# Optimization experiments

Measured on AMD Instinct MI355X. Metric: run time of the kernel, lower is better.

Reference implementation:

```python
import jax, jax.numpy as jnp
import numpy as np
import math

CHUNK = 256
NUM_HEADS = 4
EPS = 1e-5


def setup_inputs() -> dict:
    key = jax.random.key(0)
    ks = jax.random.split(key, 12)
    B, N, F = 4, 2048, 256
    x = jax.random.normal(ks[0], (B, N, F), dtype=jnp.float32)
    adj_matrix = jax.random.randint(ks[1], (N, N), 0, 2, dtype=jnp.int32)
    s = 1.0 / math.sqrt(F)
    Wq = jax.random.normal(ks[2], (F, F), dtype=jnp.float32) * s
    bq = jnp.zeros((F,), dtype=jnp.float32)
    Wk = jax.random.normal(ks[3], (F, F), dtype=jnp.float32) * s
    bk = jnp.zeros((F,), dtype=jnp.float32)
    Wv = jax.random.normal(ks[4], (F, F), dtype=jnp.float32) * s
    bv = jnp.zeros((F,), dtype=jnp.float32)
    Wo = jax.random.normal(ks[5], (F, F), dtype=jnp.float32) * s
    bo = jnp.zeros((F,), dtype=jnp.float32)
    gamma = jnp.ones((F,), dtype=jnp.float32)
    beta = jnp.zeros((F,), dtype=jnp.float32)
    return {"x": x, "adj_matrix": adj_matrix, "Wq": Wq, "bq": bq, "Wk": Wk,
            "bk": bk, "Wv": Wv, "bv": bv, "Wo": Wo, "bo": bo,
            "gamma": gamma, "beta": beta}


def reference(x, adj_matrix, Wq, bq, Wk, bk, Wv, bv, Wo, bo, gamma, beta):
    B, N, Fin = x.shape
    H = NUM_HEADS
    Dout = Wq.shape[0]
    Dh = Dout // H
    Nc = N // CHUNK  # number of key chunks

    # projections -> [B, H, N, Dh]
    q = (x @ Wq.T + bq).reshape(B, N, H, Dh).transpose(0, 2, 1, 3)
    k = (x @ Wk.T + bk).reshape(B, N, H, Dh).transpose(0, 2, 1, 3)
    v = (x @ Wv.T + bv).reshape(B, N, H, Dh).transpose(0, 2, 1, 3)

    # key/value chunks: [B, H, Nc, CHUNK, Dh]
    kc = k.reshape(B, H, Nc, CHUNK, Dh)
    vc = v.reshape(B, H, Nc, CHUNK, Dh)

    # scores per key chunk: [B, H, N, Nc, CHUNK]
    scores = jnp.einsum('bhnd,bhjcd->bhnjc', q, kc) / jnp.sqrt(
        jnp.asarray(Dh, dtype=q.dtype))
    scores = jnp.clip(scores, -10.0, 10.0)
    # adjacency mask, chunked along keys: [1, 1, N, Nc, CHUNK]
    mask = adj_matrix.reshape(N, Nc, CHUNK)[None, None]
    scores = jnp.where(mask == 0, jnp.asarray(-10.0, scores.dtype), scores)

    # FAITHFUL quirk: softmax is taken per key chunk (last axis only) and the
    # per-chunk contexts are SUMMED -> total attention mass per query is Nc.
    attn = jax.nn.softmax(scores, axis=-1)
    ctx = jnp.einsum('bhnjc,bhjcd->bhnd', attn, vc)  # sum over chunks j

    ctx = ctx.transpose(0, 2, 1, 3).reshape(B, N, Dout)
    out = ctx @ Wo.T + bo
    out = out + x  # residual (in_features == out_features)

    mu = jnp.mean(out, axis=-1, keepdims=True)
    var = jnp.mean(jnp.square(out - mu), axis=-1, keepdims=True)
    out = (out - mu) * jax.lax.rsqrt(var + EPS) * gamma + beta
    return out
```

## Files before the change

kernel.cpp:

```cpp
#include <hip/hip_runtime.h>
#include <math.h>

#define B_     4
#define N_     2048
#define F_     256
#define H_     4
#define DH     64
#define BN     8192
#define SP     72
#define SPO2   264
#define SPW    264

#define QSCALE 0.18033688011112042f
#define CLIP   14.426950408889634f

typedef _Float16 f16;
typedef _Float16 half8  __attribute__((ext_vector_type(8)));
typedef _Float16 half4v __attribute__((ext_vector_type(4)));
typedef float    floatx4 __attribute__((ext_vector_type(4)));
typedef unsigned long long u64;

__global__ __launch_bounds__(256) void prep_kernel(
    const int* __restrict__ adj, u64* __restrict__ P,
    const float* __restrict__ x,  f16* __restrict__ xh,
    const float* __restrict__ Wq, f16* __restrict__ Wqh,
    const float* __restrict__ Wk, f16* __restrict__ Wkh,
    const float* __restrict__ Wv, f16* __restrict__ Wvh,
    const float* __restrict__ Wo, f16* __restrict__ Woh)
{
    const int bid = blockIdx.x;
    if (bid < 16384) {
        const int row   = bid >> 3;
        const int chunk = bid & 7;
        const int wave  = threadIdx.x >> 6, lane = threadIdx.x & 63;
        const int key   = chunk * 256 + wave * 64 + lane;
        u64 m = __ballot(adj[(size_t)row * N_ + key] != 0);
        if (lane == 0) P[(size_t)row * 32 + chunk * 4 + wave] = m;
        return;
    }
    const float* src; f16* dst; int base;
    if      (bid < 16448) { src = Wo; dst = Woh; base = (bid - 16384) * 1024; }
    else if (bid < 16512) { src = Wq; dst = Wqh; base = (bid - 16448) * 1024; }
    else if (bid < 16576) { src = Wk; dst = Wkh; base = (bid - 16512) * 1024; }
    else if (bid < 16640) { src = Wv; dst = Wvh; base = (bid - 16576) * 1024; }
    else                  { src = x;  dst = xh;  base = (bid - 16640) * 1024; }
    const int idx = base + threadIdx.x * 4;
    float4 v = *(const float4*)(src + idx);
    half4v h; h[0] = (f16)v.x; h[1] = (f16)v.y; h[2] = (f16)v.z; h[3] = (f16)v.w;
    *(half4v*)(dst + idx) = h;
}

__global__ __launch_bounds__(512) void proj_mfma(
    const f16* __restrict__ xh,
    const f16* __restrict__ Wqh, const f16* __restrict__ Wkh, const f16* __restrict__ Wvh,
    const float* __restrict__ bq, const float* __restrict__ bk, const float* __restrict__ bv,
    f16* __restrict__ Qh, f16* __restrict__ Kh, f16* __restrict__ Vt)
{
    const int which = blockIdx.y;
    const f16*   W    = which == 0 ? Wqh : which == 1 ? Wkh : Wvh;
    const float* bias = which == 0 ? bq  : which == 1 ? bk  : bv;

    const int r0 = blockIdx.x * 64;
    const int tid  = threadIdx.x;
    const int wave = tid >> 6, lane = tid & 63;
    const int quad = lane >> 4, l16 = lane & 15;
    const int rw = wave & 3, cw = wave >> 2;

    __shared__ f16 smem[(64 + 256) * SP];
    f16* xs = smem;
    f16* wt = smem + 64 * SP;

    floatx4 zz = {0.f, 0.f, 0.f, 0.f};
    floatx4 acc[8] = {zz, zz, zz, zz, zz, zz, zz, zz};

    const int xrow = tid >> 3, xseg = (tid & 7) * 8;
    const int wrow = tid >> 1, wh = (tid & 1) * 32;

    for (int f0 = 0; f0 < F_; f0 += 64) {
        const f16* xsrc = xh + (size_t)(r0 + xrow) * F_ + f0 + xseg;
        const f16* wsrc = W  + (size_t)wrow * F_ + f0 + wh;
        float4 xa  = *(const float4*)(xsrc);
        float4 wa0 = *(const float4*)(wsrc),      wa1 = *(const float4*)(wsrc + 8);
        float4 wa2 = *(const float4*)(wsrc + 16), wa3 = *(const float4*)(wsrc + 24);
        __syncthreads();
        *(float4*)&xs[xrow * SP + xseg]   = xa;
        *(float4*)&wt[wrow * SP + wh]      = wa0;
        *(float4*)&wt[wrow * SP + wh + 8]  = wa1;
        *(float4*)&wt[wrow * SP + wh + 16] = wa2;
        *(float4*)&wt[wrow * SP + wh + 24] = wa3;
        __syncthreads();
        half8 a0 = *(const half8*)&xs[(rw * 16 + l16) * SP + quad * 8];
        half8 a1 = *(const half8*)&xs[(rw * 16 + l16) * SP + 32 + quad * 8];
#pragma unroll
        for (int ot = 0; ot < 8; ot++) {
            const int o = cw * 128 + ot * 16 + l16;
            half8 b0 = *(const half8*)&wt[o * SP + quad * 8];
            half8 b1 = *(const half8*)&wt[o * SP + 32 + quad * 8];
            acc[ot] = __builtin_amdgcn_mfma_f32_16x16x32_f16(a0, b0, acc[ot], 0, 0, 0);
            acc[ot] = __builtin_amdgcn_mfma_f32_16x16x32_f16(a1, b1, acc[ot], 0, 0, 0);
        }
    }

    const int bb = r0 >> 11, nn0 = r0 & (N_ - 1);

    if (which == 2) {
#pragma unroll
        for (int ot = 0; ot < 8; ot++) {
            const int o  = cw * 128 + ot * 16 + l16;
            const int hy = o >> 6, dh = o & 63;
            const float bv_ = bias[o];
            half4v h4;
#pragma unroll
            for (int r = 0; r < 4; r++) h4[r] = (f16)(acc[ot][r] + bv_);
            *(half4v*)(Vt + (((size_t)bb * H_ + hy) * DH + dh) * N_
                          + nn0 + rw * 16 + quad * 4) = h4;
        }
    } else {
        const float scl = (which == 0) ? QSCALE : 1.0f;
        f16* dst = which == 0 ? Qh : Kh;
        __syncthreads();
        f16* outb = smem;
#pragma unroll
        for (int ot = 0; ot < 8; ot++) {
            const int o = cw * 128 + ot * 16 + l16;
            const float bv_ = bias[o];
#pragma unroll
            for (int r = 0; r < 4; r++)
                outb[(rw * 16 + quad * 4 + r) * SPO2 + o] =
                    (f16)((acc[ot][r] + bv_) * scl);
        }
        __syncthreads();
        const int grow = tid >> 3, gseg = tid & 7;
        const int hh = gseg >> 1, dcol = (gseg & 1) * 32;
        f16* g = dst + (((size_t)bb * H_ + hh) * N_ + nn0 + grow) * DH + dcol;
        const f16* s = &outb[grow * SPO2 + gseg * 32];
#pragma unroll
        for (int k = 0; k < 4; k++)
            *(float4*)(g + k * 8) = *(const float4*)(s + k * 8);
    }
}

__global__ __launch_bounds__(256) void attn_mfma(
    const f16* __restrict__ Qh, const f16* __restrict__ Kh,
    const f16* __restrict__ Vt, const u64* __restrict__ Padj,
    f16* __restrict__ CTXP)
{
    const int nt = blockIdx.x & 15;
    const int sp = blockIdx.x >> 4;
    const int qb = nt * 128;
    const int h  = blockIdx.y;
    const int b  = blockIdx.z;
    const int bh = b * H_ + h;
    const int tid  = threadIdx.x;
    const int wave = tid >> 6, lane = tid & 63;
    const int quad = lane >> 4, l16 = lane & 15;

    __shared__ f16 QPs[128 * SP];
    __shared__ f16 Ks[64 * SP];
    __shared__ f16 Vs[64 * SP];

    {
        const int qrow = tid >> 1, qhalf = (tid & 1) * 32;
        const f16* src = Qh + ((size_t)bh * N_ + qb + qrow) * DH + qhalf;
#pragma unroll
        for (int k = 0; k < 4; k++)
            *(float4*)&QPs[qrow * SP + qhalf + k * 8] = *(const float4*)(src + k * 8);
    }
    __syncthreads();
    const half8 qf0a = *(const half8*)&QPs[(wave * 32 + l16) * SP + quad * 8];
    const half8 qf1a = *(const half8*)&QPs[(wave * 32 + l16) * SP + 32 + quad * 8];
    const half8 qf0b = *(const half8*)&QPs[(wave * 32 + 16 + l16) * SP + quad * 8];
    const half8 qf1b = *(const half8*)&QPs[(wave * 32 + 16 + l16) * SP + 32 + quad * 8];
    f16* Ps = QPs + wave * 32 * SP;

    const int qgA = qb + wave * 32 + l16;
    const int qgB = qgA + 16;
    const u64* arowA = Padj + (size_t)qgA * 32;
    const u64* arowB = Padj + (size_t)qgB * 32;

    floatx4 zz = {0.f, 0.f, 0.f, 0.f};
    floatx4 totA[4] = {zz, zz, zz, zz}, totB[4] = {zz, zz, zz, zz};

    const int kvr = tid >> 2, kvs = (tid & 3) * 16;

    for (int ci = 0; ci < 2; ci++) {
        const int c = sp * 2 + ci;
        floatx4 chA[4] = {zz, zz, zz, zz}, chB[4] = {zz, zz, zz, zz};
        float rsA = 0.f, rsB = 0.f;

        for (int kt = 0; kt < 4; kt++) {
            const int k0 = c * 256 + kt * 64;
            const f16* ksrc = Kh + ((size_t)bh * N_ + k0 + kvr) * DH + kvs;
            const f16* vsrc = Vt + ((size_t)bh * DH + kvr) * N_ + k0 + kvs;
            float4 ka0 = *(const float4*)(ksrc), ka1 = *(const float4*)(ksrc + 8);
            float4 va0 = *(const float4*)(vsrc), va1 = *(const float4*)(vsrc + 8);
            __syncthreads();
            *(float4*)&Ks[kvr * SP + kvs]     = ka0;
            *(float4*)&Ks[kvr * SP + kvs + 8] = ka1;
            *(float4*)&Vs[kvr * SP + kvs]     = va0;
            *(float4*)&Vs[kvr * SP + kvs + 8] = va1;
            __syncthreads();

            const u64 awA = arowA[k0 >> 6];
            const u64 awB = arowB[k0 >> 6];
            float rA = 0.f, rB = 0.f;
#pragma unroll
            for (int m = 0; m < 4; m++) {
                half8 a0 = *(const half8*)&Ks[(m * 16 + l16) * SP + quad * 8];
                half8 a1 = *(const half8*)&Ks[(m * 16 + l16) * SP + 32 + quad * 8];
                floatx4 sA = zz, sB = zz;
                sA = __builtin_amdgcn_mfma_f32_16x16x32_f16(a0, qf0a, sA, 0, 0, 0);
                sA = __builtin_amdgcn_mfma_f32_16x16x32_f16(a1, qf1a, sA, 0, 0, 0);
                sB = __builtin_amdgcn_mfma_f32_16x16x32_f16(a0, qf0b, sB, 0, 0, 0);
                sB = __builtin_amdgcn_mfma_f32_16x16x32_f16(a1, qf1b, sB, 0, 0, 0);
                const unsigned int nibA = (unsigned int)(awA >> (m * 16 + quad * 4)) & 0xFu;
                const unsigned int nibB = (unsigned int)(awB >> (m * 16 + quad * 4)) & 0xFu;
                half4v pA, pB;
#pragma unroll
                for (int r = 0; r < 4; r++) {
                    float svA = fminf(fmaxf(sA[r], -CLIP), CLIP);
                    svA = ((nibA >> r) & 1u) ? svA : -CLIP;
                    const float eA = __builtin_amdgcn_exp2f(svA);
                    rA += eA; pA[r] = (f16)eA;
                    float svB = fminf(fmaxf(sB[r], -CLIP), CLIP);
                    svB = ((nibB >> r) & 1u) ? svB : -CLIP;
                    const float eB = __builtin_amdgcn_exp2f(svB);
                    rB += eB; pB[r] = (f16)eB;
                }
                *(half4v*)&Ps[l16 * SP + m * 16 + quad * 4]        = pA;
                *(half4v*)&Ps[(16 + l16) * SP + m * 16 + quad * 4] = pB;
            }
            rA += __shfl_xor(rA, 16); rA += __shfl_xor(rA, 32); rsA += rA;
            rB += __shfl_xor(rB, 16); rB += __shfl_xor(rB, 32); rsB += rB;

            const half8 pA0 = *(const half8*)&Ps[l16 * SP + quad * 8];
            const half8 pA1 = *(const half8*)&Ps[l16 * SP + 32 + quad * 8];
            const half8 pB0 = *(const half8*)&Ps[(16 + l16) * SP + quad * 8];
            const half8 pB1 = *(const half8*)&Ps[(16 + l16) * SP + 32 + quad * 8];
#pragma unroll
            for (int m = 0; m < 4; m++) {
                half8 va8 = *(const half8*)&Vs[(m * 16 + l16) * SP + quad * 8];
                half8 vb8 = *(const half8*)&Vs[(m * 16 + l16) * SP + 32 + quad * 8];
                chA[m] = __builtin_amdgcn_mfma_f32_16x16x32_f16(va8, pA0, chA[m], 0, 0, 0);
                chA[m] = __builtin_amdgcn_mfma_f32_16x16x32_f16(vb8, pA1, chA[m], 0, 0, 0);
                chB[m] = __builtin_amdgcn_mfma_f32_16x16x32_f16(va8, pB0, chB[m], 0, 0, 0);
                chB[m] = __builtin_amdgcn_mfma_f32_16x16x32_f16(vb8, pB1, chB[m], 0, 0, 0);
            }
        }

        const float invA = 1.0f / rsA, invB = 1.0f / rsB;
#pragma unroll
        for (int m = 0; m < 4; m++)
#pragma unroll
            for (int r = 0; r < 4; r++) {
                totA[m][r] += chA[m][r] * invA;
                totB[m][r] += chB[m][r] * invB;
            }
    }

    f16* dstA = CTXP + (((size_t)sp * B_ + b) * N_ + qgA) * F_ + h * DH;
    f16* dstB = CTXP + (((size_t)sp * B_ + b) * N_ + qgB) * F_ + h * DH;
#pragma unroll
    for (int m = 0; m < 4; m++) {
        half4v hA, hB;
#pragma unroll
        for (int r = 0; r < 4; r++) { hA[r] = (f16)totA[m][r]; hB[r] = (f16)totB[m][r]; }
        *(half4v*)&dstA[m * 16 + quad * 4] = hA;
        *(half4v*)&dstB[m * 16 + quad * 4] = hB;
    }
}

__global__ __launch_bounds__(256) void out_mfma(
    const f16* __restrict__ CTXP, const float* __restrict__ x,
    const f16* __restrict__ Woh, const float* __restrict__ bo,
    const float* __restrict__ gamma, const float* __restrict__ beta,
    float* __restrict__ out)
{
    const int n0 = blockIdx.x * 16;
    const int tid  = threadIdx.x;
    const int wave = tid >> 6, lane = tid & 63;
    const int quad = lane >> 4, l16 = lane & 15;
    const int wrow = tid >> 2, wseg = tid & 3;

    __shared__ f16 cs[16 * SPW];
    __shared__ f16 wtile[256 * SP];
    __shared__ float red0[4][16], red1[4][16];

    {
        const int row = tid >> 4, c0 = (tid & 15) * 16;
        const size_t S = (size_t)BN * F_;
        const f16* p = CTXP + (size_t)(n0 + row) * F_ + c0;
#pragma unroll
        for (int g = 0; g < 2; g++) {
            half8 s0 = *(const half8*)(p + g * 8);
            half8 s1 = *(const half8*)(p + S + g * 8);
            half8 s2 = *(const half8*)(p + 2 * S + g * 8);
            half8 s3 = *(const half8*)(p + 3 * S + g * 8);
            half8 o;
#pragma unroll
            for (int e = 0; e < 8; e++)
                o[e] = (f16)(((float)s0[e] + (float)s1[e]) + ((float)s2[e] + (float)s3[e]));
            *(half8*)&cs[row * SPW + c0 + g * 8] = o;
        }
    }

    floatx4 zz = {0.f, 0.f, 0.f, 0.f};
    floatx4 acc[4] = {zz, zz, zz, zz};

#pragma unroll
    for (int f0 = 0; f0 < F_; f0 += 64) {
        __syncthreads();
#pragma unroll
        for (int rr = 0; rr < 4; rr++) {
            const int o = rr * 64 + wrow;
            const f16* src = Woh + (size_t)o * F_ + f0 + wseg * 16;
            *(float4*)&wtile[o * SP + wseg * 16]     = *(const float4*)(src);
            *(float4*)&wtile[o * SP + wseg * 16 + 8] = *(const float4*)(src + 8);
        }
        __syncthreads();
        half8 a0 = *(const half8*)&cs[l16 * SPW + f0 + quad * 8];
        half8 a1 = *(const half8*)&cs[l16 * SPW + f0 + 32 + quad * 8];
#pragma unroll
        for (int ot = 0; ot < 4; ot++) {
            const int o = wave * 64 + ot * 16 + l16;
            half8 b0 = *(const half8*)&wtile[o * SP + quad * 8];
            half8 b1 = *(const half8*)&wtile[o * SP + 32 + quad * 8];
            acc[ot] = __builtin_amdgcn_mfma_f32_16x16x32_f16(a0, b0, acc[ot], 0, 0, 0);
            acc[ot] = __builtin_amdgcn_mfma_f32_16x16x32_f16(a1, b1, acc[ot], 0, 0, 0);
        }
    }

#pragma unroll
    for (int ot = 0; ot < 4; ot++) {
        const int o = wave * 64 + ot * 16 + l16;
        const float bo_ = bo[o];
#pragma unroll
        for (int r = 0; r < 4; r++)
            acc[ot][r] += bo_ + x[(size_t)(n0 + quad * 4 + r) * F_ + o];
    }

#pragma unroll
    for (int r = 0; r < 4; r++) {
        float s = (acc[0][r] + acc[1][r]) + (acc[2][r] + acc[3][r]);
        float q = (acc[0][r] * acc[0][r] + acc[1][r] * acc[1][r]) +
                  (acc[2][r] * acc[2][r] + acc[3][r] * acc[3][r]);
        s += __shfl_xor(s, 1); q += __shfl_xor(q, 1);
        s += __shfl_xor(s, 2); q += __shfl_xor(q, 2);
        s += __shfl_xor(s, 4); q += __shfl_xor(q, 4);
        s += __shfl_xor(s, 8); q += __shfl_xor(q, 8);
        if (l16 == 0) { red0[wave][quad * 4 + r] = s; red1[wave][quad * 4 + r] = q; }
    }
    __syncthreads();

#pragma unroll
    for (int r = 0; r < 4; r++) {
        const int rr = quad * 4 + r;
        const float S  = (red0[0][rr] + red0[1][rr]) + (red0[2][rr] + red0[3][rr]);
        const float Q2 = (red1[0][rr] + red1[1][rr]) + (red1[2][rr] + red1[3][rr]);
        const float mu  = S * (1.0f / F_);
        const float var = Q2 * (1.0f / F_) - mu * mu;
        const float inv = rsqrtf(var + 1e-5f);
#pragma unroll
        for (int ot = 0; ot < 4; ot++) {
            const int o = wave * 64 + ot * 16 + l16;
            out[(size_t)(n0 + rr) * F_ + o] =
                (acc[ot][r] - mu) * inv * gamma[o] + beta[o];
        }
    }
}

extern "C" void kernel_launch(void* const* d_in, const int* in_sizes, int n_in,
                              void* d_out, int out_size, void* d_ws, size_t ws_size,
                              hipStream_t stream)
{
    const float* x     = (const float*)d_in[0];
    const int*   adj   = (const int*)  d_in[1];
    const float* Wq    = (const float*)d_in[2];
    const float* bq    = (const float*)d_in[3];
    const float* Wk    = (const float*)d_in[4];
    const float* bk    = (const float*)d_in[5];
    const float* Wv    = (const float*)d_in[6];
    const float* bv    = (const float*)d_in[7];
    const float* Wo    = (const float*)d_in[8];
    const float* bo    = (const float*)d_in[9];
    const float* gamma = (const float*)d_in[10];
    const float* beta  = (const float*)d_in[11];
    float* out = (float*)d_out;

    float* ws = (float*)d_ws;
    f16*   CTXP = (f16*)(ws);
    f16*   Qh   = (f16*)(ws + 4194304);
    f16*   Kh   = (f16*)(ws + 5242880);
    f16*   Vt   = (f16*)(ws + 6291456);
    u64*   Padj = (u64*)(ws + 7340032);
    f16*   Woh  = (f16*)(ws + 7471104);
    f16*   xh   = CTXP;
    f16*   Wqh  = (f16*)(ws + 1048576);
    f16*   Wkh  = (f16*)(ws + 1081344);
    f16*   Wvh  = (f16*)(ws + 1114112);

    hipLaunchKernelGGL(prep_kernel, dim3(18688), dim3(256), 0, stream,
                       adj, Padj, x, xh, Wq, Wqh, Wk, Wkh, Wv, Wvh, Wo, Woh);
    hipLaunchKernelGGL(proj_mfma, dim3(BN / 64, 3), dim3(512), 0, stream,
                       xh, Wqh, Wkh, Wvh, bq, bk, bv, Qh, Kh, Vt);
    hipLaunchKernelGGL(attn_mfma, dim3(64, H_, B_), dim3(256), 0, stream,
                       Qh, Kh, Vt, Padj, CTXP);
    hipLaunchKernelGGL(out_mfma, dim3(BN / 16), dim3(256), 0, stream,
                       CTXP, x, Woh, bo, gamma, beta, out);
}
```

Measured before the change: 163.4 us.

## Fuse prep into projection kernel and split attention into one chunk per block

```diff
diff --git a/kernel.cpp b/kernel.cpp
--- a/kernel.cpp
+++ b/kernel.cpp
@@ -20,48 +20,46 @@
 typedef float    floatx4 __attribute__((ext_vector_type(4)));
 typedef unsigned long long u64;
 
-__global__ __launch_bounds__(256) void prep_kernel(
-    const int* __restrict__ adj, u64* __restrict__ P,
-    const float* __restrict__ x,  f16* __restrict__ xh,
-    const float* __restrict__ Wq, f16* __restrict__ Wqh,
-    const float* __restrict__ Wk, f16* __restrict__ Wkh,
-    const float* __restrict__ Wv, f16* __restrict__ Wvh,
-    const float* __restrict__ Wo, f16* __restrict__ Woh)
+__device__ __forceinline__ half8 cvt8(float4 a, float4 b) {
+    half8 h;
+    h[0] = (f16)a.x; h[1] = (f16)a.y; h[2] = (f16)a.z; h[3] = (f16)a.w;
+    h[4] = (f16)b.x; h[5] = (f16)b.y; h[6] = (f16)b.z; h[7] = (f16)b.w;
+    return h;
+}
+
+__global__ __launch_bounds__(512) void proj_fused(
+    const float* __restrict__ x,
+    const float* __restrict__ Wq, const float* __restrict__ Wk, const float* __restrict__ Wv,
+    const float* __restrict__ bq, const float* __restrict__ bk, const float* __restrict__ bv,
+    const int* __restrict__ adj, u64* __restrict__ Padj,
+    const float* __restrict__ Wo, f16* __restrict__ Woh,
+    f16* __restrict__ Qh, f16* __restrict__ Kh, f16* __restrict__ Vt)
 {
     const int bid = blockIdx.x;
-    if (bid < 16384) {
-        const int row   = bid >> 3;
-        const int chunk = bid & 7;
-        const int wave  = threadIdx.x >> 6, lane = threadIdx.x & 63;
-        const int key   = chunk * 256 + wave * 64 + lane;
+    const int tid = threadIdx.x;
+
+    if (bid >= 416) {
+        const int idx = bid - 416;
+        const int row = idx >> 2, seg = idx & 3;
+        const int wave = tid >> 6, lane = tid & 63;
+        const int key = seg * 512 + wave * 64 + lane;
         u64 m = __ballot(adj[(size_t)row * N_ + key] != 0);
-        if (lane == 0) P[(size_t)row * 32 + chunk * 4 + wave] = m;
+        if (lane == 0) Padj[(size_t)row * 32 + seg * 8 + wave] = m;
         return;
     }
-    const float* src; f16* dst; int base;
-    if      (bid < 16448) { src = Wo; dst = Woh; base = (bid - 16384) * 1024; }
-    else if (bid < 16512) { src = Wq; dst = Wqh; base = (bid - 16448) * 1024; }
-    else if (bid < 16576) { src = Wk; dst = Wkh; base = (bid - 16512) * 1024; }
-    else if (bid < 16640) { src = Wv; dst = Wvh; base = (bid - 16576) * 1024; }
-    else                  { src = x;  dst = xh;  base = (bid - 16640) * 1024; }
-    const int idx = base + threadIdx.x * 4;
-    float4 v = *(const float4*)(src + idx);
-    half4v h; h[0] = (f16)v.x; h[1] = (f16)v.y; h[2] = (f16)v.z; h[3] = (f16)v.w;
-    *(half4v*)(dst + idx) = h;
-}
-
-__global__ __launch_bounds__(512) void proj_mfma(
-    const f16* __restrict__ xh,
-    const f16* __restrict__ Wqh, const f16* __restrict__ Wkh, const f16* __restrict__ Wvh,
-    const float* __restrict__ bq, const float* __restrict__ bk, const float* __restrict__ bv,
-    f16* __restrict__ Qh, f16* __restrict__ Kh, f16* __restrict__ Vt)
-{
-    const int which = blockIdx.y;
-    const f16*   W    = which == 0 ? Wqh : which == 1 ? Wkh : Wvh;
-    const float* bias = which == 0 ? bq  : which == 1 ? bk  : bv;
-
-    const int r0 = blockIdx.x * 64;
-    const int tid  = threadIdx.x;
+    if (bid >= 384) {
+        const int idx = (bid - 384) * 2048 + tid * 4;
+        float4 v = *(const float4*)(Wo + idx);
+        half4v h; h[0] = (f16)v.x; h[1] = (f16)v.y; h[2] = (f16)v.z; h[3] = (f16)v.w;
+        *(half4v*)(Woh + idx) = h;
+        return;
+    }
+
+    const int which = bid >> 7;
+    const float* W    = which == 0 ? Wq : which == 1 ? Wk : Wv;
+    const float* bias = which == 0 ? bq : which == 1 ? bk : bv;
+
+    const int r0 = (bid & 127) * 64;
     const int wave = tid >> 6, lane = tid & 63;
     const int quad = lane >> 4, l16 = lane & 15;
     const int rw = wave & 3, cw = wave >> 2;
@@ -77,17 +75,19 @@
     const int wrow = tid >> 1, wh = (tid & 1) * 32;
 
     for (int f0 = 0; f0 < F_; f0 += 64) {
-        const f16* xsrc = xh + (size_t)(r0 + xrow) * F_ + f0 + xseg;
-        const f16* wsrc = W  + (size_t)wrow * F_ + f0 + wh;
-        float4 xa  = *(const float4*)(xsrc);
-        float4 wa0 = *(const float4*)(wsrc),      wa1 = *(const float4*)(wsrc + 8);
-        float4 wa2 = *(const float4*)(wsrc + 16), wa3 = *(const float4*)(wsrc + 24);
-        __syncthreads();
-        *(float4*)&xs[xrow * SP + xseg]   = xa;
-        *(float4*)&wt[wrow * SP + wh]      = wa0;
-        *(float4*)&wt[wrow * SP + wh + 8]  = wa1;
-        *(float4*)&wt[wrow * SP + wh + 16] = wa2;
-        *(float4*)&wt[wrow * SP + wh + 24] = wa3;
+        const float* xsrc = x + (size_t)(r0 + xrow) * F_ + f0 + xseg;
+        const float* wsrc = W + (size_t)wrow * F_ + f0 + wh;
+        float4 xa0 = *(const float4*)(xsrc), xa1 = *(const float4*)(xsrc + 4);
+        float4 w0 = *(const float4*)(wsrc),      w1 = *(const float4*)(wsrc + 4);
+        float4 w2 = *(const float4*)(wsrc + 8),  w3 = *(const float4*)(wsrc + 12);
+        float4 w4 = *(const float4*)(wsrc + 16), w5 = *(const float4*)(wsrc + 20);
+        float4 w6 = *(const float4*)(wsrc + 24), w7 = *(const float4*)(wsrc + 28);
+        __syncthreads();
+        *(half8*)&xs[xrow * SP + xseg]     = cvt8(xa0, xa1);
+        *(half8*)&wt[wrow * SP + wh]       = cvt8(w0, w1);
+        *(half8*)&wt[wrow * SP + wh + 8]   = cvt8(w2, w3);
+        *(half8*)&wt[wrow * SP + wh + 16]  = cvt8(w4, w5);
+        *(half8*)&wt[wrow * SP + wh + 24]  = cvt8(w6, w7);
         __syncthreads();
         half8 a0 = *(const half8*)&xs[(rw * 16 + l16) * SP + quad * 8];
         half8 a1 = *(const half8*)&xs[(rw * 16 + l16) * SP + 32 + quad * 8];
@@ -179,92 +179,82 @@
     const u64* arowB = Padj + (size_t)qgB * 32;
 
     floatx4 zz = {0.f, 0.f, 0.f, 0.f};
-    floatx4 totA[4] = {zz, zz, zz, zz}, totB[4] = {zz, zz, zz, zz};
+    floatx4 chA[4] = {zz, zz, zz, zz}, chB[4] = {zz, zz, zz, zz};
+    float rsA = 0.f, rsB = 0.f;
 
     const int kvr = tid >> 2, kvs = (tid & 3) * 16;
 
-    for (int ci = 0; ci < 2; ci++) {
-        const int c = sp * 2 + ci;
-        floatx4 chA[4] = {zz, zz, zz, zz}, chB[4] = {zz, zz, zz, zz};
-        float rsA = 0.f, rsB = 0.f;
-
-        for (int kt = 0; kt < 4; kt++) {
-            const int k0 = c * 256 + kt * 64;
-            const f16* ksrc = Kh + ((size_t)bh * N_ + k0 + kvr) * DH + kvs;
-            const f16* vsrc = Vt + ((size_t)bh * DH + kvr) * N_ + k0 + kvs;
-            float4 ka0 = *(const float4*)(ksrc), ka1 = *(const float4*)(ksrc + 8);
-            float4 va0 = *(const float4*)(vsrc), va1 = *(const float4*)(vsrc + 8);
-            __syncthreads();
-            *(float4*)&Ks[kvr * SP + kvs]     = ka0;
-            *(float4*)&Ks[kvr * SP + kvs + 8] = ka1;
-            *(float4*)&Vs[kvr * SP + kvs]     = va0;
-            *(float4*)&Vs[kvr * SP + kvs + 8] = va1;
-            __syncthreads();
-
-            const u64 awA = arowA[k0 >> 6];
-            const u64 awB = arowB[k0 >> 6];
-            float rA = 0.f, rB = 0.f;
-#pragma unroll
-            for (int m = 0; m < 4; m++) {
-                half8 a0 = *(const half8*)&Ks[(m * 16 + l16) * SP + quad * 8];
-                half8 a1 = *(const half8*)&Ks[(m * 16 + l16) * SP + 32 + quad * 8];
-                floatx4 sA = zz, sB = zz;
-                sA = __builtin_amdgcn_mfma_f32_16x16x32_f16(a0, qf0a, sA, 0, 0, 0);
-                sA = __builtin_amdgcn_mfma_f32_16x16x32_f16(a1, qf1a, sA, 0, 0, 0);
-                sB = __builtin_amdgcn_mfma_f32_16x16x32_f16(a0, qf0b, sB, 0, 0, 0);
-                sB = __builtin_amdgcn_mfma_f32_16x16x32_f16(a1, qf1b, sB, 0, 0, 0);
-                const unsigned int nibA = (unsigned int)(awA >> (m * 16 + quad * 4)) & 0xFu;
-                const unsigned int nibB = (unsigned int)(awB >> (m * 16 + quad * 4)) & 0xFu;
-                half4v pA, pB;
-#pragma unroll
-                for (int r = 0; r < 4; r++) {
-                    float svA = fminf(fmaxf(sA[r], -CLIP), CLIP);
-                    svA = ((nibA >> r) & 1u) ? svA : -CLIP;
-                    const float eA = __builtin_amdgcn_exp2f(svA);
-                    rA += eA; pA[r] = (f16)eA;
-                    float svB = fminf(fmaxf(sB[r], -CLIP), CLIP);
-                    svB = ((nibB >> r) & 1u) ? svB : -CLIP;
-                    const float eB = __builtin_amdgcn_exp2f(svB);
-                    rB += eB; pB[r] = (f16)eB;
-                }
-                *(half4v*)&Ps[l16 * SP + m * 16 + quad * 4]        = pA;
-                *(half4v*)&Ps[(16 + l16) * SP + m * 16 + quad * 4] = pB;
+    for (int kt = 0; kt < 4; kt++) {
+        const int k0 = sp * 256 + kt * 64;
+        const f16* ksrc = Kh + ((size_t)bh * N_ + k0 + kvr) * DH + kvs;
+        const f16* vsrc = Vt + ((size_t)bh * DH + kvr) * N_ + k0 + kvs;
+        float4 ka0 = *(const float4*)(ksrc), ka1 = *(const float4*)(ksrc + 8);
+        float4 va0 = *(const float4*)(vsrc), va1 = *(const float4*)(vsrc + 8);
+        __syncthreads();
+        *(float4*)&Ks[kvr * SP + kvs]     = ka0;
+        *(float4*)&Ks[kvr * SP + kvs + 8] = ka1;
+        *(float4*)&Vs[kvr * SP + kvs]     = va0;
+        *(float4*)&Vs[kvr * SP + kvs + 8] = va1;
+        __syncthreads();
+
+        const u64 awA = arowA[k0 >> 6];
+        const u64 awB = arowB[k0 >> 6];
+        float rA = 0.f, rB = 0.f;
+#pragma unroll
+        for (int m = 0; m < 4; m++) {
+            half8 a0 = *(const half8*)&Ks[(m * 16 + l16) * SP + quad * 8];
+            half8 a1 = *(const half8*)&Ks[(m * 16 + l16) * SP + 32 + quad * 8];
+            floatx4 sA = zz, sB = zz;
+            sA = __builtin_amdgcn_mfma_f32_16x16x32_f16(a0, qf0a, sA, 0, 0, 0);
+            sA = __builtin_amdgcn_mfma_f32_16x16x32_f16(a1, qf1a, sA, 0, 0, 0);
+            sB = __builtin_amdgcn_mfma_f32_16x16x32_f16(a0, qf0b, sB, 0, 0, 0);
+            sB = __builtin_amdgcn_mfma_f32_16x16x32_f16(a1, qf1b, sB, 0, 0, 0);
+            const unsigned int nibA = (unsigned int)(awA >> (m * 16 + quad * 4)) & 0xFu;
+            const unsigned int nibB = (unsigned int)(awB >> (m * 16 + quad * 4)) & 0xFu;
+            half4v pA, pB;
+#pragma unroll
+            for (int r = 0; r < 4; r++) {
+                float svA = fminf(fmaxf(sA[r], -CLIP), CLIP);
+                svA = ((nibA >> r) & 1u) ? svA : -CLIP;
+                const float eA = __builtin_amdgcn_exp2f(svA);
+                rA += eA; pA[r] = (f16)eA;
+                float svB = fminf(fmaxf(sB[r], -CLIP), CLIP);
+                svB = ((nibB >> r) & 1u) ? svB : -CLIP;
+                const float eB = __builtin_amdgcn_exp2f(svB);
+                rB += eB; pB[r] = (f16)eB;
             }
-            rA += __shfl_xor(rA, 16); rA += __shfl_xor(rA, 32); rsA += rA;
-            rB += __shfl_xor(rB, 16); rB += __shfl_xor(rB, 32); rsB += rB;
-
-            const half8 pA0 = *(const half8*)&Ps[l16 * SP + quad * 8];
-            const half8 pA1 = *(const half8*)&Ps[l16 * SP + 32 + quad * 8];
-            const half8 pB0 = *(const half8*)&Ps[(16 + l16) * SP + quad * 8];
-            const half8 pB1 = *(const half8*)&Ps[(16 + l16) * SP + 32 + quad * 8];
-#pragma unroll
-            for (int m = 0; m < 4; m++) {
-                half8 va8 = *(const half8*)&Vs[(m * 16 + l16) * SP + quad * 8];
-                half8 vb8 = *(const half8*)&Vs[(m * 16 + l16) * SP + 32 + quad * 8];
-                chA[m] = __builtin_amdgcn_mfma_f32_16x16x32_f16(va8, pA0, chA[m], 0, 0, 0);
-                chA[m] = __builtin_amdgcn_mfma_f32_16x16x32_f16(vb8, pA1, chA[m], 0, 0, 0);
-                chB[m] = __builtin_amdgcn_mfma_f32_16x16x32_f16(va8, pB0, chB[m], 0, 0, 0);
-                chB[m] = __builtin_amdgcn_mfma_f32_16x16x32_f16(vb8, pB1, chB[m], 0, 0, 0);
-            }
-        }
-
-        const float invA = 1.0f / rsA, invB = 1.0f / rsB;
-#pragma unroll
-        for (int m = 0; m < 4; m++)
-#pragma unroll
-            for (int r = 0; r < 4; r++) {
-                totA[m][r] += chA[m][r] * invA;
-                totB[m][r] += chB[m][r] * invB;
-            }
-    }
-
+            *(half4v*)&Ps[l16 * SP + m * 16 + quad * 4]        = pA;
+            *(half4v*)&Ps[(16 + l16) * SP + m * 16 + quad * 4] = pB;
+        }
+        rA += __shfl_xor(rA, 16); rA += __shfl_xor(rA, 32); rsA += rA;
+        rB += __shfl_xor(rB, 16); rB += __shfl_xor(rB, 32); rsB += rB;
+
+        const half8 pA0 = *(const half8*)&Ps[l16 * SP + quad * 8];
+        const half8 pA1 = *(const half8*)&Ps[l16 * SP + 32 + quad * 8];
+        const half8 pB0 = *(const half8*)&Ps[(16 + l16) * SP + quad * 8];
+        const half8 pB1 = *(const half8*)&Ps[(16 + l16) * SP + 32 + quad * 8];
+#pragma unroll
+        for (int m = 0; m < 4; m++) {
+            half8 va8 = *(const half8*)&Vs[(m * 16 + l16) * SP + quad * 8];
+            half8 vb8 = *(const half8*)&Vs[(m * 16 + l16) * SP + 32 + quad * 8];
+            chA[m] = __builtin_amdgcn_mfma_f32_16x16x32_f16(va8, pA0, chA[m], 0, 0, 0);
+            chA[m] = __builtin_amdgcn_mfma_f32_16x16x32_f16(vb8, pA1, chA[m], 0, 0, 0);
+            chB[m] = __builtin_amdgcn_mfma_f32_16x16x32_f16(va8, pB0, chB[m], 0, 0, 0);
+            chB[m] = __builtin_amdgcn_mfma_f32_16x16x32_f16(vb8, pB1, chB[m], 0, 0, 0);
+        }
+    }
+
+    const float invA = 1.0f / rsA, invB = 1.0f / rsB;
     f16* dstA = CTXP + (((size_t)sp * B_ + b) * N_ + qgA) * F_ + h * DH;
     f16* dstB = CTXP + (((size_t)sp * B_ + b) * N_ + qgB) * F_ + h * DH;
 #pragma unroll
     for (int m = 0; m < 4; m++) {
         half4v hA, hB;
 #pragma unroll
-        for (int r = 0; r < 4; r++) { hA[r] = (f16)totA[m][r]; hB[r] = (f16)totB[m][r]; }
+        for (int r = 0; r < 4; r++) {
+            hA[r] = (f16)(chA[m][r] * invA);
+            hB[r] = (f16)(chB[m][r] * invB);
+        }
         *(half4v*)&dstA[m * 16 + quad * 4] = hA;
         *(half4v*)&dstB[m * 16 + quad * 4] = hB;
     }
@@ -292,14 +282,16 @@
         const f16* p = CTXP + (size_t)(n0 + row) * F_ + c0;
 #pragma unroll
         for (int g = 0; g < 2; g++) {
-            half8 s0 = *(const half8*)(p + g * 8);
-            half8 s1 = *(const half8*)(p + S + g * 8);
-            half8 s2 = *(const half8*)(p + 2 * S + g * 8);
-            half8 s3 = *(const half8*)(p + 3 * S + g * 8);
+            float v[8] = {0.f,0.f,0.f,0.f,0.f,0.f,0.f,0.f};
+#pragma unroll
+            for (int pp = 0; pp < 8; pp++) {
+                half8 s = *(const half8*)(p + (size_t)pp * S + g * 8);
+#pragma unroll
+                for (int e = 0; e < 8; e++) v[e] += (float)s[e];
+            }
             half8 o;
 #pragma unroll
-            for (int e = 0; e < 8; e++)
-                o[e] = (f16)(((float)s0[e] + (float)s1[e]) + ((float)s2[e] + (float)s3[e]));
+            for (int e = 0; e < 8; e++) o[e] = (f16)v[e];
             *(half8*)&cs[row * SPW + c0 + g * 8] = o;
         }
     }
@@ -389,21 +381,15 @@
 
     float* ws = (float*)d_ws;
     f16*   CTXP = (f16*)(ws);
-    f16*   Qh   = (f16*)(ws + 4194304);
-    f16*   Kh   = (f16*)(ws + 5242880);
-    f16*   Vt   = (f16*)(ws + 6291456);
-    u64*   Padj = (u64*)(ws + 7340032);
-    f16*   Woh  = (f16*)(ws + 7471104);
-    f16*   xh   = CTXP;
-    f16*   Wqh  = (f16*)(ws + 1048576);
-    f16*   Wkh  = (f16*)(ws + 1081344);
-    f16*   Wvh  = (f16*)(ws + 1114112);
-
-    hipLaunchKernelGGL(prep_kernel, dim3(18688), dim3(256), 0, stream,
-                       adj, Padj, x, xh, Wq, Wqh, Wk, Wkh, Wv, Wvh, Wo, Woh);
-    hipLaunchKernelGGL(proj_mfma, dim3(BN / 64, 3), dim3(512), 0, stream,
-                       xh, Wqh, Wkh, Wvh, bq, bk, bv, Qh, Kh, Vt);
-    hipLaunchKernelGGL(attn_mfma, dim3(64, H_, B_), dim3(256), 0, stream,
+    f16*   Qh   = (f16*)(ws + 8388608);
+    f16*   Kh   = (f16*)(ws + 9437184);
+    f16*   Vt   = (f16*)(ws + 10485760);
+    u64*   Padj = (u64*)(ws + 11534336);
+    f16*   Woh  = (f16*)(ws + 11665408);
+
+    hipLaunchKernelGGL(proj_fused, dim3(8608), dim3(512), 0, stream,
+                       x, Wq, Wk, Wv, bq, bk, bv, adj, Padj, Wo, Woh, Qh, Kh, Vt);
+    hipLaunchKernelGGL(attn_mfma, dim3(128, H_, B_), dim3(256), 0, stream,
                        Qh, Kh, Vt, Padj, CTXP);
     hipLaunchKernelGGL(out_mfma, dim3(BN / 16), dim3(256), 0, stream,
                        CTXP, x, Woh, bo, gamma, beta, out);
```

Measured after the change: 163.2 us. Within noise of the previous version (-0.2%).
